# Kernel tuning notes

Hardware: AMD Instinct MI355X
Metric: run time of the kernel (lower is better)

Reference implementation:

```python
import jax, jax.numpy as jnp
import numpy as np

KV_SIZE = 960
NUM_HEADS = 4
EPS = 1e-5  # InstanceNorm2d default eps
CHANNELS = [64, 128, 256, 512]
B, N = 8, 1024


def setup_inputs() -> dict:
    key = jax.random.key(0)
    ks = jax.random.split(key, 16)
    inp = {
        'emb1': jax.random.normal(ks[0], (B, N, 64), jnp.float32),
        'emb2': jax.random.normal(ks[1], (B, N, 128), jnp.float32),
        'emb3': jax.random.normal(ks[2], (B, N, 256), jnp.float32),
        'emb4': jax.random.normal(ks[3], (B, N, 512), jnp.float32),
        'emb_all': jax.random.normal(ks[4], (B, N, KV_SIZE), jnp.float32),
    }
    w = 0.02  # weight init scale
    inp['Wq1'] = jax.random.normal(ks[5], (NUM_HEADS, 64, 64), jnp.float32) * w
    inp['Wq2'] = jax.random.normal(ks[6], (NUM_HEADS, 128, 128), jnp.float32) * w
    inp['Wq3'] = jax.random.normal(ks[7], (NUM_HEADS, 256, 256), jnp.float32) * w
    inp['Wq4'] = jax.random.normal(ks[8], (NUM_HEADS, 512, 512), jnp.float32) * w
    inp['Wk'] = jax.random.normal(ks[9], (NUM_HEADS, KV_SIZE, KV_SIZE), jnp.float32) * w
    inp['Wv'] = jax.random.normal(ks[10], (NUM_HEADS, KV_SIZE, KV_SIZE), jnp.float32) * w
    inp['Wo1'] = jax.random.normal(ks[11], (64, 64), jnp.float32) * w
    inp['Wo2'] = jax.random.normal(ks[12], (128, 128), jnp.float32) * w
    inp['Wo3'] = jax.random.normal(ks[13], (256, 256), jnp.float32) * w
    inp['Wo4'] = jax.random.normal(ks[14], (512, 512), jnp.float32) * w
    return inp


def _branch(emb, Wq, K, V, Wo):
    # per-head query projection (Linear: x @ W^T), stacked over heads -> [B,H,N,C]
    Q = jnp.einsum('bnc,hdc->bhnd', emb, Wq)
    # Q^T @ K -> channel-channel scores [B,H,C,KV]
    scores = jnp.einsum('bhnc,bhnk->bhck', Q, K) / np.float32(np.sqrt(KV_SIZE))
    # InstanceNorm2d over (C,KV) per (batch, head), no affine
    mu = scores.mean(axis=(2, 3), keepdims=True)
    var = scores.var(axis=(2, 3), keepdims=True)
    scores = (scores - mu) * jax.lax.rsqrt(var + EPS)
    probs = jax.nn.softmax(scores, axis=-1)  # softmax over KV axis
    # probs @ V^T -> [B,H,C,N]; mean over heads fused into the contraction
    ctx = jnp.einsum('bhck,bhnk->bcn', probs, V) / np.float32(NUM_HEADS)
    ctx = ctx.transpose(0, 2, 1)  # [B,N,C]
    return ctx @ Wo.T  # output projection (dropout=0 -> identity)


def reference(emb1, emb2, emb3, emb4, emb_all,
              Wq1, Wq2, Wq3, Wq4, Wk, Wv, Wo1, Wo2, Wo3, Wo4):
    # shared K/V over the concatenated-channel embedding, per head: [B,H,N,KV]
    K = jnp.einsum('bnk,hok->bhno', emb_all, Wk)
    V = jnp.einsum('bnk,hok->bhno', emb_all, Wv)
    O1 = _branch(emb1, Wq1, K, V, Wo1)
    O2 = _branch(emb2, Wq2, K, V, Wo2)
    O3 = _branch(emb3, Wq3, K, V, Wo3)
    O4 = _branch(emb4, Wq4, K, V, Wo4)
    return (O1, O2, O3, O4)
```

## Files before the change

kernel.cpp:

```cpp
#include <hip/hip_runtime.h>
#include <hip/hip_bf16.h>

typedef __attribute__((ext_vector_type(8))) short short8;
typedef __attribute__((ext_vector_type(4))) float f32x4;

static __device__ __forceinline__ unsigned short f2bf(float x) {
  union { __hip_bfloat16 h; unsigned short u; } cv;
  cv.h = __float2bfloat16(x);
  return cv.u;
}
static __device__ __forceinline__ float bf2f(unsigned short u) {
  union { unsigned int u; float f; } cv;
  cv.u = ((unsigned int)u) << 16;
  return cv.f;
}

static __device__ __forceinline__ void xcd_swizzle(unsigned& bx, unsigned& by, unsigned& bz) {
  unsigned nwg = gridDim.x * gridDim.y * gridDim.z;
  unsigned lin = blockIdx.x + gridDim.x * (blockIdx.y + gridDim.y * blockIdx.z);
  unsigned chunk = nwg >> 3;
  lin = (lin & 7) * chunk + (lin >> 3);
  bx = lin % gridDim.x;
  unsigned tmp = lin / gridDim.x;
  by = tmp % gridDim.y;
  bz = tmp / gridDim.y;
}

__global__ void cast4_kernel(const float* __restrict__ s0, long n0,
                             const float* __restrict__ s1, long n1,
                             const float* __restrict__ s2, long n2,
                             const float* __restrict__ s3, long n3,
                             unsigned short* __restrict__ dst) {
  long N4 = (n0 + n1 + n2 + n3) >> 2;
  for (long i = blockIdx.x * (long)blockDim.x + threadIdx.x; i < N4;
       i += (long)gridDim.x * blockDim.x) {
    long e = i << 2;
    const float* s; long j = e;
    if (j < n0) s = s0;
    else { j -= n0; if (j < n1) s = s1;
      else { j -= n1; if (j < n2) s = s2;
        else { j -= n2; s = s3; } } }
    float4 v = *reinterpret_cast<const float4*>(s + j);
    ushort4 o;
    o.x = f2bf(v.x); o.y = f2bf(v.y); o.z = f2bf(v.z); o.w = f2bf(v.w);
    *reinterpret_cast<ushort4*>(dst + e) = o;
  }
}

__global__ __launch_bounds__(256)
void tcast_kernel(const float* __restrict__ in, unsigned short* __restrict__ out,
                  int R, int C, long sIn, long sOut) {
  __shared__ float tile[64][65];
  int z = blockIdx.z;
  const float* src = in + (long)z * sIn;
  unsigned short* dst = out + (long)z * sOut;
  int r0 = blockIdx.y * 64, c0 = blockIdx.x * 64;
  int t = threadIdx.x;
  int lr = t >> 4;
  int lc = (t & 15) * 4;
#pragma unroll
  for (int j = 0; j < 4; ++j) {
    int r = lr + j * 16;
    float4 v = *reinterpret_cast<const float4*>(src + (long)(r0 + r) * C + c0 + lc);
    tile[r][lc] = v.x; tile[r][lc + 1] = v.y; tile[r][lc + 2] = v.z; tile[r][lc + 3] = v.w;
  }
  __syncthreads();
#pragma unroll
  for (int j = 0; j < 4; ++j) {
    int oc = lr + j * 16;
    ushort4 o;
    o.x = f2bf(tile[lc][oc]);
    o.y = f2bf(tile[lc + 1][oc]);
    o.z = f2bf(tile[lc + 2][oc]);
    o.w = f2bf(tile[lc + 3][oc]);
    *reinterpret_cast<ushort4*>(dst + (long)(c0 + oc) * R + r0 + lc) = o;
  }
}

struct YDesc { int m0[8]; int mw[8]; int br[8]; };

template<int TM, int TN, int OUT, int DO_STATS, int YD>
__global__ __launch_bounds__(256)
void gemm_nt(const unsigned short* __restrict__ A,
             const unsigned short* __restrict__ B,
             void* __restrict__ Cp,
             int K, int lda, int ldb, long ldc, int Hdiv,
             long sAb, long sAh, long sBb, long sBh, long sC,
             float alpha, float* __restrict__ stats,
             int Mclamp, int Nclamp, int Mwrite, int Nwrite, int Nvalid, YDesc yd) {
  constexpr int WM = TM / 32, WN = TN / 32;
  __shared__ unsigned short As[TM * 32];
  __shared__ unsigned short Bs[TN * 32];
  __shared__ float red[8];

  unsigned bxu, byu, bzu;
  xcd_swizzle(bxu, byu, bzu);
  int z = (int)bzu;
  int b = z / Hdiv, h = z % Hdiv;
  const unsigned short* Ab = A + (long)b * sAb + (long)h * sAh;
  const unsigned short* Bb = B + (long)b * sBb + (long)h * sBh;
  int y = (int)byu;
  int m0 = YD ? yd.m0[y] : y * TM;
  int rowLimit = YD ? (m0 + yd.mw[y]) : Mwrite;
  int n0 = (int)bxu * TN;
  int t = threadIdx.x;
  int lane = t & 63, wave = t >> 6;
  int wm = (wave >> 1) * (TM / 2), wn = (wave & 1) * (TN / 2);
  int l15 = lane & 15, q = lane >> 4;
  int arow = t >> 2, acol = (t & 3) * 8;

  int rA[TM / 64], rB[TN / 64];
#pragma unroll
  for (int r = 0; r < TM / 64; ++r) rA[r] = min(m0 + r * 64 + arow, Mclamp - 1);
#pragma unroll
  for (int r = 0; r < TN / 64; ++r) rB[r] = min(n0 + r * 64 + arow, Nclamp - 1);

  f32x4 acc[WM][WN] = {};

  for (int k0 = 0; k0 < K; k0 += 32) {
    __syncthreads();
#pragma unroll
    for (int r = 0; r < TM / 64; ++r)
      __builtin_amdgcn_global_load_lds(
          (const __attribute__((address_space(1))) void*)(Ab + (long)rA[r] * lda + acol + k0),
          (__attribute__((address_space(3))) void*)(As + r * 2048 + t * 8), 16, 0, 0);
#pragma unroll
    for (int r = 0; r < TN / 64; ++r)
      __builtin_amdgcn_global_load_lds(
          (const __attribute__((address_space(1))) void*)(Bb + (long)rB[r] * ldb + acol + k0),
          (__attribute__((address_space(3))) void*)(Bs + r * 2048 + t * 8), 16, 0, 0);
    __syncthreads();
    short8 af[WM], bfr[WN];
#pragma unroll
    for (int i = 0; i < WM; ++i)
      af[i] = *reinterpret_cast<const short8*>(As + (wm + i * 16 + l15) * 32 + q * 8);
#pragma unroll
    for (int j = 0; j < WN; ++j)
      bfr[j] = *reinterpret_cast<const short8*>(Bs + (wn + j * 16 + l15) * 32 + q * 8);
#pragma unroll
    for (int i = 0; i < WM; ++i)
#pragma unroll
      for (int j = 0; j < WN; ++j)
        acc[i][j] = __builtin_amdgcn_mfma_f32_16x16x32_bf16(af[i], bfr[j], acc[i][j], 0, 0, 0);
  }

  long cbase = (long)z * sC;
  float ssum = 0.f, ssq = 0.f;
#pragma unroll
  for (int i = 0; i < WM; ++i)
#pragma unroll
    for (int j = 0; j < WN; ++j)
#pragma unroll
      for (int r = 0; r < 4; ++r) {
        float v = acc[i][j][r] * alpha;
        int rg = m0 + wm + i * 16 + q * 4 + r;
        int cg = n0 + wn + j * 16 + l15;
        if (rg < rowLimit && cg < Nwrite) {
          long idx = cbase + (long)rg * ldc + cg;
          if (OUT == 1) ((float*)Cp)[idx] = v;
          else if (OUT == 2) ((_Float16*)Cp)[idx] = (_Float16)v;
          else ((unsigned short*)Cp)[idx] = f2bf(v);
        }
        if (DO_STATS && rg < rowLimit && cg < Nvalid) { ssum += v; ssq += v * v; }
      }

  if (DO_STATS) {
#pragma unroll
    for (int o = 32; o; o >>= 1) {
      ssum += __shfl_down(ssum, o, 64);
      ssq  += __shfl_down(ssq,  o, 64);
    }
    if (lane == 0) { red[wave] = ssum; red[wave + 4] = ssq; }
    __syncthreads();
    if (t == 0) {
      long slot = YD ? ((long)z * 8 + yd.br[y] * 2) : ((long)z * 2);
      atomicAdd(stats + slot,     red[0] + red[1] + red[2] + red[3]);
      atomicAdd(stats + slot + 1, red[4] + red[5] + red[6] + red[7]);
    }
  }
}

struct BDesc { int K[8]; int aRow0[8]; int out0[8]; int mw[8]; int bc[8]; long aOff[8]; long aH[8]; };

__global__ __launch_bounds__(256)
void gemm_bd(const unsigned short* __restrict__ A0,
             const unsigned short* __restrict__ B0,
             unsigned short* __restrict__ Cp,
             int ldb, long sBz, long sC, BDesc d) {
  constexpr int TM = 128, TN = 64, WM = 4, WN = 2;
  __shared__ unsigned short As[TM * 32];
  __shared__ unsigned short Bs[TN * 32];
  unsigned bxu, byu, bzu;
  xcd_swizzle(bxu, byu, bzu);
  int z = (int)bzu;
  int b = z >> 2, h = z & 3;
  int y = (int)byu;
  int K = d.K[y];
  const unsigned short* Ab = A0 + d.aOff[y] + (long)h * d.aH[y];
  const unsigned short* Bb = B0 + (long)b * sBz + d.bc[y];
  int n0 = (int)bxu * TN;
  int t = threadIdx.x;
  int lane = t & 63, wave = t >> 6;
  int wm = (wave >> 1) * 64, wn = (wave & 1) * 32;
  int l15 = lane & 15, q = lane >> 4;
  int arow = t >> 2, acol = (t & 3) * 8;

  int rA0 = min(d.aRow0[y] + arow, K - 1);
  int rA1 = min(d.aRow0[y] + 64 + arow, K - 1);
  int rB0 = n0 + arow;

  f32x4 acc[WM][WN] = {};
  for (int k0 = 0; k0 < K; k0 += 32) {
    __syncthreads();
    __builtin_amdgcn_global_load_lds(
        (const __attribute__((address_space(1))) void*)(Ab + (long)rA0 * K + acol + k0),
        (__attribute__((address_space(3))) void*)(As + t * 8), 16, 0, 0);
    __builtin_amdgcn_global_load_lds(
        (const __attribute__((address_space(1))) void*)(Ab + (long)rA1 * K + acol + k0),
        (__attribute__((address_space(3))) void*)(As + 2048 + t * 8), 16, 0, 0);
    __builtin_amdgcn_global_load_lds(
        (const __attribute__((address_space(1))) void*)(Bb + (long)rB0 * ldb + acol + k0),
        (__attribute__((address_space(3))) void*)(Bs + t * 8), 16, 0, 0);
    __syncthreads();
    short8 af[WM], bfr[WN];
#pragma unroll
    for (int i = 0; i < WM; ++i)
      af[i] = *reinterpret_cast<const short8*>(As + (wm + i * 16 + l15) * 32 + q * 8);
#pragma unroll
    for (int j = 0; j < WN; ++j)
      bfr[j] = *reinterpret_cast<const short8*>(Bs + (wn + j * 16 + l15) * 32 + q * 8);
#pragma unroll
    for (int i = 0; i < WM; ++i)
#pragma unroll
      for (int j = 0; j < WN; ++j)
        acc[i][j] = __builtin_amdgcn_mfma_f32_16x16x32_bf16(af[i], bfr[j], acc[i][j], 0, 0, 0);
  }

  long cbase = (long)z * sC;
  int mw = d.mw[y], out0 = d.out0[y];
#pragma unroll
  for (int i = 0; i < WM; ++i)
#pragma unroll
    for (int j = 0; j < WN; ++j)
#pragma unroll
      for (int r = 0; r < 4; ++r) {
        int loc = wm + i * 16 + q * 4 + r;
        int cg = n0 + wn + j * 16 + l15;
        if (loc < mw) {
          long idx = cbase + (long)(out0 + loc) * 960 + cg;
          Cp[idx] = f2bf(acc[i][j][r]);
        }
      }
}

__global__ __launch_bounds__(256)
void norm_softmax_all(_Float16* __restrict__ S, const float* __restrict__ stats) {
  long row = blockIdx.x;
  int z = (int)(row / 960), cc = (int)(row % 960);
  int br = (cc < 64) ? 0 : (cc < 192) ? 1 : (cc < 448) ? 2 : 3;
  int Cbr = (br == 0) ? 64 : (br == 1) ? 128 : (br == 2) ? 256 : 512;
  float invCnt = 1.0f / ((float)Cbr * 960.0f);
  float m1 = stats[z * 8 + br * 2 + 0] * invCnt;
  float m2 = stats[z * 8 + br * 2 + 1] * invCnt;
  float rsig = rsqrtf(m2 - m1 * m1 + 1e-5f);
  _Float16* s = S + row * 960;
  int t = threadIdx.x;
  float e[4]; float acc = 0.f;
#pragma unroll
  for (int j = 0; j < 4; ++j) {
    int i = t + j * 256;
    if (i < 960) { e[j] = __expf(((float)s[i] - m1) * rsig); acc += e[j]; }
    else e[j] = 0.f;
  }
#pragma unroll
  for (int o = 32; o; o >>= 1) acc += __shfl_down(acc, o, 64);
  __shared__ float red[4];
  if ((t & 63) == 0) red[t >> 6] = acc;
  __syncthreads();
  float inv = 1.0f / (red[0] + red[1] + red[2] + red[3]);
  unsigned short* p = (unsigned short*)s;
#pragma unroll
  for (int j = 0; j < 4; ++j) {
    int i = t + j * 256;
    if (i < 960) p[i] = f2bf(e[j] * inv);
  }
}

__global__ __launch_bounds__(256)
void hreduce_k(const unsigned short* __restrict__ in, unsigned short* __restrict__ outp) {
  long g = blockIdx.x * 256L + threadIdx.x;
  long e8 = g * 8;
  long b = e8 / 921600;
  long r = e8 % 921600;
  float acc[8] = {};
#pragma unroll
  for (int h = 0; h < 4; ++h) {
    short8 v = *reinterpret_cast<const short8*>(in + (b * 4 + h) * 921600 + r);
#pragma unroll
    for (int k = 0; k < 8; ++k) acc[k] += bf2f((unsigned short)v[k]);
  }
  short8 o;
#pragma unroll
  for (int k = 0; k < 8; ++k) o[k] = (short)f2bf(acc[k] * 0.25f);
  *reinterpret_cast<short8*>(outp + e8) = o;
}

struct MDesc {
  long aOff[4], bOff[4], cOff[4];
  long sAz[4], sBz[4], sCz[4];
  long iA[4], iB[4];
  int  lda[4], ldb[4], ldcv[4];
  int  Kk[4], Ncl[4], nIn[4];
  int  nstart[4];
  float alpha[4];
};

template<int OUT_F32>
__global__ __launch_bounds__(256)
void gemm_multi(const unsigned short* __restrict__ A0,
                const unsigned short* __restrict__ B0,
                void* __restrict__ Cp, MDesc d) {
  __shared__ unsigned short As[128 * 32];
  __shared__ unsigned short Bs[128 * 32];
  unsigned bxu, byu, bzu;
  xcd_swizzle(bxu, byu, bzu);
  int bx = (int)bxu;
  int br = (bx >= d.nstart[3]) ? 3 : (bx >= d.nstart[2]) ? 2 : (bx >= d.nstart[1]) ? 1 : 0;
  int z = (int)bzu;
  int n0 = (bx - d.nstart[br]) * 128;
  int m0 = (int)byu * 128;
  int K = d.Kk[br], lda = d.lda[br], ldb = d.ldb[br], ldc = d.ldcv[br];
  int Ncl = d.Ncl[br], nInner = d.nIn[br];
  float alpha = d.alpha[br];
  const unsigned short* Ab = A0 + d.aOff[br] + (long)z * d.sAz[br];
  const unsigned short* Bb = B0 + d.bOff[br] + (long)z * d.sBz[br];

  int t = threadIdx.x, lane = t & 63, wave = t >> 6;
  int wm = (wave >> 1) * 64, wn = (wave & 1) * 64;
  int l15 = lane & 15, q = lane >> 4;
  int arow = t >> 2, acol = (t & 3) * 8;
  int rA0 = m0 + arow, rA1 = m0 + 64 + arow;
  int rB0 = min(n0 + arow, Ncl - 1), rB1 = min(n0 + 64 + arow, Ncl - 1);

  f32x4 acc[4][4] = {};
  for (int it = 0; it < nInner; ++it) {
    const unsigned short* Ait = Ab + (long)it * d.iA[br];
    const unsigned short* Bit = Bb + (long)it * d.iB[br];
    for (int k0 = 0; k0 < K; k0 += 32) {
      __syncthreads();
      __builtin_amdgcn_global_load_lds(
          (const __attribute__((address_space(1))) void*)(Ait + (long)rA0 * lda + acol + k0),
          (__attribute__((address_space(3))) void*)(As + t * 8), 16, 0, 0);
      __builtin_amdgcn_global_load_lds(
          (const __attribute__((address_space(1))) void*)(Ait + (long)rA1 * lda + acol + k0),
          (__attribute__((address_space(3))) void*)(As + 2048 + t * 8), 16, 0, 0);
      __builtin_amdgcn_global_load_lds(
          (const __attribute__((address_space(1))) void*)(Bit + (long)rB0 * ldb + acol + k0),
          (__attribute__((address_space(3))) void*)(Bs + t * 8), 16, 0, 0);
      __builtin_amdgcn_global_load_lds(
          (const __attribute__((address_space(1))) void*)(Bit + (long)rB1 * ldb + acol + k0),
          (__attribute__((address_space(3))) void*)(Bs + 2048 + t * 8), 16, 0, 0);
      __syncthreads();
      short8 af[4], bfr[4];
#pragma unroll
      for (int i = 0; i < 4; ++i)
        af[i] = *reinterpret_cast<const short8*>(As + (wm + i * 16 + l15) * 32 + q * 8);
#pragma unroll
      for (int j = 0; j < 4; ++j)
        bfr[j] = *reinterpret_cast<const short8*>(Bs + (wn + j * 16 + l15) * 32 + q * 8);
#pragma unroll
      for (int i = 0; i < 4; ++i)
#pragma unroll
        for (int j = 0; j < 4; ++j)
          acc[i][j] = __builtin_amdgcn_mfma_f32_16x16x32_bf16(af[i], bfr[j], acc[i][j], 0, 0, 0);
    }
  }

  long cb = d.cOff[br] + (long)z * d.sCz[br];
#pragma unroll
  for (int i = 0; i < 4; ++i)
#pragma unroll
    for (int j = 0; j < 4; ++j)
#pragma unroll
      for (int r = 0; r < 4; ++r) {
        float v = acc[i][j][r] * alpha;
        int rg = m0 + wm + i * 16 + q * 4 + r;
        int cg = n0 + wn + j * 16 + l15;
        if (cg < Ncl) {
          long idx = cb + (long)rg * ldc + cg;
          if (OUT_F32) ((float*)Cp)[idx] = v;
          else ((unsigned short*)Cp)[idx] = f2bf(v);
        }
      }
}

extern "C" void kernel_launch(void* const* d_in, const int* in_sizes, int n_in,
                              void* d_out, int out_size, void* d_ws, size_t ws_size,
                              hipStream_t stream) {
  const float* embs[4] = {(const float*)d_in[0], (const float*)d_in[1],
                          (const float*)d_in[2], (const float*)d_in[3]};
  const float* embA = (const float*)d_in[4];
  const float* Wq1  = (const float*)d_in[5];
  const float* Wq2  = (const float*)d_in[6];
  const float* Wq3  = (const float*)d_in[7];
  const float* Wq4  = (const float*)d_in[8];
  const float* Wk   = (const float*)d_in[9];
  const float* Wv   = (const float*)d_in[10];
  float* out = (float*)d_out;

  char* base = (char*)d_ws;
  size_t off = 0;
  auto take = [&](size_t bytes) -> void* {
    void* p = base + off;
    off += (bytes + 255) & ~(size_t)255;
    return p;
  };
  unsigned short* EA    = (unsigned short*)take(15728640);
  unsigned short* embAT = (unsigned short*)take(15728640);
  unsigned short* embTc = (unsigned short*)take(15728640);
  unsigned short* WQb   = (unsigned short*)take(2785280);
  unsigned short* WKb   = (unsigned short*)take(7372800);
  unsigned short* WvT   = (unsigned short*)take(7372800);
  unsigned short* WOb   = (unsigned short*)take(696320);
  float*          ST    = (float*)take(1024);
  unsigned short* GT    = (unsigned short*)take(14745600);
  unsigned short* Tbuf  = (unsigned short*)take(58982400);
  char*           SCr   = (char*)take(58982400);
  _Float16*       SC    = (_Float16*)SCr;
  unsigned short* PR    = (unsigned short*)SCr;
  unsigned short* SPWh  = Tbuf;
  unsigned short* SPW   = GT;
  unsigned short* CT    = embAT;

  if (ws_size < off) return;

  hipMemsetAsync(ST, 0, 1024, stream);

  const long Cs[4]     = {64, 128, 256, 512};
  const long c0s[4]    = {0, 64, 192, 448};
  const long woOff[4]  = {0, 4096, 20480, 86016};
  const long outOff[4] = {0, 524288, 1572864, 3670016};
  const float kscale = 0.0322748612f;
  YDesc ydDummy = {};

  cast4_kernel<<<4096, 256, 0, stream>>>(embA, 7864320, embA, 0, embA, 0, embA, 0, EA);
  cast4_kernel<<<1024, 256, 0, stream>>>(Wq1, 16384, Wq2, 65536, Wq3, 262144, Wq4, 1048576, WQb);
  cast4_kernel<<<1024, 256, 0, stream>>>(Wk, 3686400, Wk, 0, Wk, 0, Wk, 0, WKb);
  cast4_kernel<<<512, 256, 0, stream>>>((const float*)d_in[11], 4096, (const float*)d_in[12], 16384,
                                        (const float*)d_in[13], 65536, (const float*)d_in[14], 262144, WOb);
  tcast_kernel<<<dim3(15, 16, 8), 256, 0, stream>>>(embA, embAT, 1024, 960, 983040, 983040);
  for (int i = 0; i < 4; ++i)
    tcast_kernel<<<dim3((int)Cs[i] / 64, 16, 8), 256, 0, stream>>>(
        embs[i], embTc + c0s[i] * 1024, 1024, (int)Cs[i], 1024 * Cs[i], 983040);
  tcast_kernel<<<dim3(15, 15, 4), 256, 0, stream>>>(Wv, WvT, 960, 960, 921600, 921600);

  gemm_nt<128, 128, 0, 0, 0><<<dim3(8, 8, 8), 256, 0, stream>>>(
      embAT, embTc, GT, 1024, 1024, 1024, 960, 1,
      983040L, 0L, 983040L, 0L, 921600L,
      1.0f, nullptr, 960, 960, 960, 960, 0, ydDummy);

  {
    BDesc d;
    const int brOf[8]  = {0, 1, 2, 2, 3, 3, 3, 3};
    const int ar0[8]   = {0, 0, 0, 128, 0, 128, 256, 384};
    const long wqOff[4] = {0, 16384, 81920, 344064};
    for (int y = 0; y < 8; ++y) {
      int br = brOf[y];
      int Ci = (int)Cs[br];
      d.K[y] = Ci;
      d.aRow0[y] = ar0[y];
      d.out0[y] = (int)c0s[br] + ar0[y];
      d.mw[y] = (br == 0) ? 64 : 128;
      d.bc[y] = (int)c0s[br];
      d.aOff[y] = wqOff[br];
      d.aH[y] = (long)Ci * Ci;
    }
    gemm_bd<<<dim3(15, 8, 32), 256, 0, stream>>>(WQb, GT, Tbuf, 960, 921600L, 921600L, d);
  }

  {
    YDesc yd;
    const int m0s[8] = {0, 64, 192, 320, 448, 576, 704, 832};
    const int mws[8] = {64, 128, 128, 128, 128, 128, 128, 128};
    const int brs[8] = {0, 1, 2, 2, 3, 3, 3, 3};
    for (int y = 0; y < 8; ++y) { yd.m0[y] = m0s[y]; yd.mw[y] = mws[y]; yd.br[y] = brs[y]; }
    gemm_nt<128, 128, 2, 1, 1><<<dim3(8, 8, 32), 256, 0, stream>>>(
        Tbuf, WKb, SC, 960, 960, 960, 960, 4,
        3686400L, 921600L, 0L, 921600L, 921600L,
        kscale, ST, 960, 960, 960, 960, 960, yd);
  }

  norm_softmax_all<<<dim3(32 * 960), 256, 0, stream>>>(SC, ST);

  gemm_nt<128, 128, 0, 0, 0><<<dim3(8, 8, 32), 256, 0, stream>>>(
      PR, WvT, SPWh, 960, 960, 960, 960, 4,
      3686400L, 921600L, 0L, 921600L, 921600L,
      1.0f, nullptr, 960, 960, 960, 960, 0, ydDummy);

  hreduce_k<<<dim3(3600), 256, 0, stream>>>(SPWh, SPW);

  gemm_nt<128, 128, 0, 0, 0><<<dim3(8, 8, 8), 256, 0, stream>>>(
      EA, SPW, CT, 960, 960, 960, 960, 1,
      983040L, 0L, 921600L, 0L, 983040L,
      1.0f, nullptr, 1024, 960, 1024, 960, 0, ydDummy);

  {
    MDesc d;
    for (int i = 0; i < 4; ++i) {
      long C = Cs[i];
      d.aOff[i] = c0s[i];       d.sAz[i] = 983040L;          d.iA[i] = 0;
      d.bOff[i] = woOff[i];     d.sBz[i] = 0;                d.iB[i] = 0;
      d.cOff[i] = outOff[i];    d.sCz[i] = 1024L * C;
      d.lda[i] = 960; d.ldb[i] = (int)C; d.ldcv[i] = (int)C;
      d.Kk[i] = (int)C; d.Ncl[i] = (int)C; d.nIn[i] = 1;
      d.alpha[i] = 1.0f;
    }
    d.nstart[0] = 0; d.nstart[1] = 1; d.nstart[2] = 2; d.nstart[3] = 4;
    gemm_multi<1><<<dim3(8, 8, 8), 256, 0, stream>>>(CT, WOb, out, d);
  }
  (void)in_sizes; (void)n_in; (void)out_size;
}
```

Measured before the change: 550.6 us.

## Double-buffer LDS in GEMMs and fuse head-mean into PV GEMM

Converts the GEMM kernels to double-buffered shared memory so the next k-tile's global-to-LDS loads overlap the current tile's MFMAs, with one barrier per step instead of two. The probs·Vᵀ GEMM now loops over the four heads inside the block and applies the 0.25 scale, removing the separate head-reduce kernel and its intermediate buffer. This trades extra LDS per block and fewer blocks (longer per-block k-loops) for lower latency and less memory traffic.

After: 513.8 us. -6.7%, faster.

```diff
diff --git a/kernel.cpp b/kernel.cpp
--- a/kernel.cpp
+++ b/kernel.cpp
@@ -8,11 +8,6 @@
   union { __hip_bfloat16 h; unsigned short u; } cv;
   cv.h = __float2bfloat16(x);
   return cv.u;
-}
-static __device__ __forceinline__ float bf2f(unsigned short u) {
-  union { unsigned int u; float f; } cv;
-  cv.u = ((unsigned int)u) << 16;
-  return cv.f;
 }
 
 static __device__ __forceinline__ void xcd_swizzle(unsigned& bx, unsigned& by, unsigned& bz) {
@@ -86,11 +81,12 @@
              void* __restrict__ Cp,
              int K, int lda, int ldb, long ldc, int Hdiv,
              long sAb, long sAh, long sBb, long sBh, long sC,
+             int nInner, long iA, long iB,
              float alpha, float* __restrict__ stats,
              int Mclamp, int Nclamp, int Mwrite, int Nwrite, int Nvalid, YDesc yd) {
   constexpr int WM = TM / 32, WN = TN / 32;
-  __shared__ unsigned short As[TM * 32];
-  __shared__ unsigned short Bs[TN * 32];
+  __shared__ unsigned short As[2][TM * 32];
+  __shared__ unsigned short Bs[2][TN * 32];
   __shared__ float red[8];
 
   unsigned bxu, byu, bzu;
@@ -115,33 +111,46 @@
 #pragma unroll
   for (int r = 0; r < TN / 64; ++r) rB[r] = min(n0 + r * 64 + arow, Nclamp - 1);
 
-  f32x4 acc[WM][WN] = {};
-
-  for (int k0 = 0; k0 < K; k0 += 32) {
-    __syncthreads();
+  int kSteps = K >> 5;
+  int nt = nInner * kSteps;
+  const unsigned short* Asrc = Ab;
+  const unsigned short* Bsrc = Bb;
+  int kk = 0;
+
+  auto stage = [&](int bufSel) {
 #pragma unroll
     for (int r = 0; r < TM / 64; ++r)
       __builtin_amdgcn_global_load_lds(
-          (const __attribute__((address_space(1))) void*)(Ab + (long)rA[r] * lda + acol + k0),
-          (__attribute__((address_space(3))) void*)(As + r * 2048 + t * 8), 16, 0, 0);
+          (const __attribute__((address_space(1))) void*)(Asrc + (long)rA[r] * lda + acol + kk),
+          (__attribute__((address_space(3))) void*)(&As[bufSel][r * 2048 + t * 8]), 16, 0, 0);
 #pragma unroll
     for (int r = 0; r < TN / 64; ++r)
       __builtin_amdgcn_global_load_lds(
-          (const __attribute__((address_space(1))) void*)(Bb + (long)rB[r] * ldb + acol + k0),
-          (__attribute__((address_space(3))) void*)(Bs + r * 2048 + t * 8), 16, 0, 0);
-    __syncthreads();
+          (const __attribute__((address_space(1))) void*)(Bsrc + (long)rB[r] * ldb + acol + kk),
+          (__attribute__((address_space(3))) void*)(&Bs[bufSel][r * 2048 + t * 8]), 16, 0, 0);
+  };
+  auto advance = [&]() { kk += 32; if (kk >= K) { kk = 0; Asrc += iA; Bsrc += iB; } };
+
+  f32x4 acc[WM][WN] = {};
+  stage(0);
+  advance();
+  __syncthreads();
+  for (int s = 0; s < nt; ++s) {
+    int cur = s & 1;
+    if (s + 1 < nt) { stage(cur ^ 1); advance(); }
     short8 af[WM], bfr[WN];
 #pragma unroll
     for (int i = 0; i < WM; ++i)
-      af[i] = *reinterpret_cast<const short8*>(As + (wm + i * 16 + l15) * 32 + q * 8);
+      af[i] = *reinterpret_cast<const short8*>(&As[cur][(wm + i * 16 + l15) * 32 + q * 8]);
 #pragma unroll
     for (int j = 0; j < WN; ++j)
-      bfr[j] = *reinterpret_cast<const short8*>(Bs + (wn + j * 16 + l15) * 32 + q * 8);
+      bfr[j] = *reinterpret_cast<const short8*>(&Bs[cur][(wn + j * 16 + l15) * 32 + q * 8]);
 #pragma unroll
     for (int i = 0; i < WM; ++i)
 #pragma unroll
       for (int j = 0; j < WN; ++j)
         acc[i][j] = __builtin_amdgcn_mfma_f32_16x16x32_bf16(af[i], bfr[j], acc[i][j], 0, 0, 0);
+    __syncthreads();
   }
 
   long cbase = (long)z * sC;
@@ -188,8 +197,8 @@
              unsigned short* __restrict__ Cp,
              int ldb, long sBz, long sC, BDesc d) {
   constexpr int TM = 128, TN = 64, WM = 4, WN = 2;
-  __shared__ unsigned short As[TM * 32];
-  __shared__ unsigned short Bs[TN * 32];
+  __shared__ unsigned short As[2][TM * 32];
+  __shared__ unsigned short Bs[2][TN * 32];
   unsigned bxu, byu, bzu;
   xcd_swizzle(bxu, byu, bzu);
   int z = (int)bzu;
@@ -209,31 +218,40 @@
   int rA1 = min(d.aRow0[y] + 64 + arow, K - 1);
   int rB0 = n0 + arow;
 
+  int kk = 0;
+  auto stage = [&](int bufSel) {
+    __builtin_amdgcn_global_load_lds(
+        (const __attribute__((address_space(1))) void*)(Ab + (long)rA0 * K + acol + kk),
+        (__attribute__((address_space(3))) void*)(&As[bufSel][t * 8]), 16, 0, 0);
+    __builtin_amdgcn_global_load_lds(
+        (const __attribute__((address_space(1))) void*)(Ab + (long)rA1 * K + acol + kk),
+        (__attribute__((address_space(3))) void*)(&As[bufSel][2048 + t * 8]), 16, 0, 0);
+    __builtin_amdgcn_global_load_lds(
+        (const __attribute__((address_space(1))) void*)(Bb + (long)rB0 * ldb + acol + kk),
+        (__attribute__((address_space(3))) void*)(&Bs[bufSel][t * 8]), 16, 0, 0);
+  };
+
+  int nt = K >> 5;
   f32x4 acc[WM][WN] = {};
-  for (int k0 = 0; k0 < K; k0 += 32) {
-    __syncthreads();
-    __builtin_amdgcn_global_load_lds(
-        (const __attribute__((address_space(1))) void*)(Ab + (long)rA0 * K + acol + k0),
-        (__attribute__((address_space(3))) void*)(As + t * 8), 16, 0, 0);
-    __builtin_amdgcn_global_load_lds(
-        (const __attribute__((address_space(1))) void*)(Ab + (long)rA1 * K + acol + k0),
-        (__attribute__((address_space(3))) void*)(As + 2048 + t * 8), 16, 0, 0);
-    __builtin_amdgcn_global_load_lds(
-        (const __attribute__((address_space(1))) void*)(Bb + (long)rB0 * ldb + acol + k0),
-        (__attribute__((address_space(3))) void*)(Bs + t * 8), 16, 0, 0);
-    __syncthreads();
+  stage(0);
+  kk += 32;
+  __syncthreads();
+  for (int s = 0; s < nt; ++s) {
+    int cur = s & 1;
+    if (s + 1 < nt) { stage(cur ^ 1); kk += 32; }
     short8 af[WM], bfr[WN];
 #pragma unroll
     for (int i = 0; i < WM; ++i)
-      af[i] = *reinterpret_cast<const short8*>(As + (wm + i * 16 + l15) * 32 + q * 8);
+      af[i] = *reinterpret_cast<const short8*>(&As[cur][(wm + i * 16 + l15) * 32 + q * 8]);
 #pragma unroll
     for (int j = 0; j < WN; ++j)
-      bfr[j] = *reinterpret_cast<const short8*>(Bs + (wn + j * 16 + l15) * 32 + q * 8);
+      bfr[j] = *reinterpret_cast<const short8*>(&Bs[cur][(wn + j * 16 + l15) * 32 + q * 8]);
 #pragma unroll
     for (int i = 0; i < WM; ++i)
 #pragma unroll
       for (int j = 0; j < WN; ++j)
         acc[i][j] = __builtin_amdgcn_mfma_f32_16x16x32_bf16(af[i], bfr[j], acc[i][j], 0, 0, 0);
+    __syncthreads();
   }
 
   long cbase = (long)z * sC;
@@ -286,25 +304,6 @@
   }
 }
 
-__global__ __launch_bounds__(256)
-void hreduce_k(const unsigned short* __restrict__ in, unsigned short* __restrict__ outp) {
-  long g = blockIdx.x * 256L + threadIdx.x;
-  long e8 = g * 8;
-  long b = e8 / 921600;
-  long r = e8 % 921600;
-  float acc[8] = {};
-#pragma unroll
-  for (int h = 0; h < 4; ++h) {
-    short8 v = *reinterpret_cast<const short8*>(in + (b * 4 + h) * 921600 + r);
-#pragma unroll
-    for (int k = 0; k < 8; ++k) acc[k] += bf2f((unsigned short)v[k]);
-  }
-  short8 o;
-#pragma unroll
-  for (int k = 0; k < 8; ++k) o[k] = (short)f2bf(acc[k] * 0.25f);
-  *reinterpret_cast<short8*>(outp + e8) = o;
-}
-
 struct MDesc {
   long aOff[4], bOff[4], cOff[4];
   long sAz[4], sBz[4], sCz[4];
@@ -320,8 +319,8 @@
 void gemm_multi(const unsigned short* __restrict__ A0,
                 const unsigned short* __restrict__ B0,
                 void* __restrict__ Cp, MDesc d) {
-  __shared__ unsigned short As[128 * 32];
-  __shared__ unsigned short Bs[128 * 32];
+  __shared__ unsigned short As[2][128 * 32];
+  __shared__ unsigned short Bs[2][128 * 32];
   unsigned bxu, byu, bzu;
   xcd_swizzle(bxu, byu, bzu);
   int bx = (int)bxu;
@@ -331,6 +330,7 @@
   int m0 = (int)byu * 128;
   int K = d.Kk[br], lda = d.lda[br], ldb = d.ldb[br], ldc = d.ldcv[br];
   int Ncl = d.Ncl[br], nInner = d.nIn[br];
+  long iA = d.iA[br], iB = d.iB[br];
   float alpha = d.alpha[br];
   const unsigned short* Ab = A0 + d.aOff[br] + (long)z * d.sAz[br];
   const unsigned short* Bb = B0 + d.bOff[br] + (long)z * d.sBz[br];
@@ -342,38 +342,46 @@
   int rA0 = m0 + arow, rA1 = m0 + 64 + arow;
   int rB0 = min(n0 + arow, Ncl - 1), rB1 = min(n0 + 64 + arow, Ncl - 1);
 
+  const unsigned short* Asrc = Ab;
+  const unsigned short* Bsrc = Bb;
+  int kk = 0;
+  auto stage = [&](int bufSel) {
+    __builtin_amdgcn_global_load_lds(
+        (const __attribute__((address_space(1))) void*)(Asrc + (long)rA0 * lda + acol + kk),
+        (__attribute__((address_space(3))) void*)(&As[bufSel][t * 8]), 16, 0, 0);
+    __builtin_amdgcn_global_load_lds(
+        (const __attribute__((address_space(1))) void*)(Asrc + (long)rA1 * lda + acol + kk),
+        (__attribute__((address_space(3))) void*)(&As[bufSel][2048 + t * 8]), 16, 0, 0);
+    __builtin_amdgcn_global_load_lds(
+        (const __attribute__((address_space(1))) void*)(Bsrc + (long)rB0 * ldb + acol + kk),
+        (__attribute__((address_space(3))) void*)(&Bs[bufSel][t * 8]), 16, 0, 0);
+    __builtin_amdgcn_global_load_lds(
+        (const __attribute__((address_space(1))) void*)(Bsrc + (long)rB1 * ldb + acol + kk),
+        (__attribute__((address_space(3))) void*)(&Bs[bufSel][2048 + t * 8]), 16, 0, 0);
+  };
+  auto advance = [&]() { kk += 32; if (kk >= K) { kk = 0; Asrc += iA; Bsrc += iB; } };
+
+  int nt = nInner * (K >> 5);
   f32x4 acc[4][4] = {};
-  for (int it = 0; it < nInner; ++it) {
-    const unsigned short* Ait = Ab + (long)it * d.iA[br];
-    const unsigned short* Bit = Bb + (long)it * d.iB[br];
-    for (int k0 = 0; k0 < K; k0 += 32) {
-      __syncthreads();
-      __builtin_amdgcn_global_load_lds(
-          (const __attribute__((address_space(1))) void*)(Ait + (long)rA0 * lda + acol + k0),
-          (__attribute__((address_space(3))) void*)(As + t * 8), 16, 0, 0);
-      __builtin_amdgcn_global_load_lds(
-          (const __attribute__((address_space(1))) void*)(Ait + (long)rA1 * lda + acol + k0),
-          (__attribute__((address_space(3))) void*)(As + 2048 + t * 8), 16, 0, 0);
-      __builtin_amdgcn_global_load_lds(
-          (const __attribute__((address_space(1))) void*)(Bit + (long)rB0 * ldb + acol + k0),
-          (__attribute__((address_space(3))) void*)(Bs + t * 8), 16, 0, 0);
-      __builtin_amdgcn_global_load_lds(
-          (const __attribute__((address_space(1))) void*)(Bit + (long)rB1 * ldb + acol + k0),
-          (__attribute__((address_space(3))) void*)(Bs + 2048 + t * 8), 16, 0, 0);
-      __syncthreads();
-      short8 af[4], bfr[4];
-#pragma unroll
-      for (int i = 0; i < 4; ++i)
-        af[i] = *reinterpret_cast<const short8*>(As + (wm + i * 16 + l15) * 32 + q * 8);
+  stage(0);
+  advance();
+  __syncthreads();
+  for (int s = 0; s < nt; ++s) {
+    int cur = s & 1;
+    if (s + 1 < nt) { stage(cur ^ 1); advance(); }
+    short8 af[4], bfr[4];
+#pragma unroll
+    for (int i = 0; i < 4; ++i)
+      af[i] = *reinterpret_cast<const short8*>(&As[cur][(wm + i * 16 + l15) * 32 + q * 8]);
+#pragma unroll
+    for (int j = 0; j < 4; ++j)
+      bfr[j] = *reinterpret_cast<const short8*>(&Bs[cur][(wn + j * 16 + l15) * 32 + q * 8]);
+#pragma unroll
+    for (int i = 0; i < 4; ++i)
 #pragma unroll
       for (int j = 0; j < 4; ++j)
-        bfr[j] = *reinterpret_cast<const short8*>(Bs + (wn + j * 16 + l15) * 32 + q * 8);
-#pragma unroll
-      for (int i = 0; i < 4; ++i)
-#pragma unroll
-        for (int j = 0; j < 4; ++j)
-          acc[i][j] = __builtin_amdgcn_mfma_f32_16x16x32_bf16(af[i], bfr[j], acc[i][j], 0, 0, 0);
-    }
+        acc[i][j] = __builtin_amdgcn_mfma_f32_16x16x32_bf16(af[i], bfr[j], acc[i][j], 0, 0, 0);
+    __syncthreads();
   }
 
   long cb = d.cOff[br] + (long)z * d.sCz[br];
@@ -428,7 +436,6 @@
   char*           SCr   = (char*)take(58982400);
   _Float16*       SC    = (_Float16*)SCr;
   unsigned short* PR    = (unsigned short*)SCr;
-  unsigned short* SPWh  = Tbuf;
   unsigned short* SPW   = GT;
   unsigned short* CT    = embAT;
 
@@ -457,7 +464,7 @@
   gemm_nt<128, 128, 0, 0, 0><<<dim3(8, 8, 8), 256, 0, stream>>>(
       embAT, embTc, GT, 1024, 1024, 1024, 960, 1,
       983040L, 0L, 983040L, 0L, 921600L,
-      1.0f, nullptr, 960, 960, 960, 960, 0, ydDummy);
+      1, 0L, 0L, 1.0f, nullptr, 960, 960, 960, 960, 0, ydDummy);
 
   {
     BDesc d;
@@ -487,22 +494,20 @@
     gemm_nt<128, 128, 2, 1, 1><<<dim3(8, 8, 32), 256, 0, stream>>>(
         Tbuf, WKb, SC, 960, 960, 960, 960, 4,
         3686400L, 921600L, 0L, 921600L, 921600L,
-        kscale, ST, 960, 960, 960, 960, 960, yd);
+        1, 0L, 0L, kscale, ST, 960, 960, 960, 960, 960, yd);
   }
 
   norm_softmax_all<<<dim3(32 * 960), 256, 0, stream>>>(SC, ST);
 
-  gemm_nt<128, 128, 0, 0, 0><<<dim3(8, 8, 32), 256, 0, stream>>>(
-      PR, WvT, SPWh, 960, 960, 960, 960, 4,
-      3686400L, 921600L, 0L, 921600L, 921600L,
-      1.0f, nullptr, 960, 960, 960, 960, 0, ydDummy);
-
-  hreduce_k<<<dim3(3600), 256, 0, stream>>>(SPWh, SPW);
+  gemm_nt<128, 128, 0, 0, 0><<<dim3(8, 8, 8), 256, 0, stream>>>(
+      PR, WvT, SPW, 960, 960, 960, 960, 1,
+      3686400L, 0L, 0L, 0L, 921600L,
+      4, 921600L, 921600L, 0.25f, nullptr, 960, 960, 960, 960, 0, ydDummy);
 
   gemm_nt<128, 128, 0, 0, 0><<<dim3(8, 8, 8), 256, 0, stream>>>(
       EA, SPW, CT, 960, 960, 960, 960, 1,
       983040L, 0L, 921600L, 0L, 983040L,
-      1.0f, nullptr, 1024, 960, 1024, 960, 0, ydDummy);
+      1, 0L, 0L, 1.0f, nullptr, 1024, 960, 1024, 960, 0, ydDummy);
 
   {
     MDesc d;
```
